# Optimization experiments

Hardware: AMD Instinct MI355X
Metric: run time of the kernel (lower is better)

## Reference

```python
import math
import jax, jax.numpy as jnp
import numpy as np

BLOCKSIZE = 1024  # Hadamard block length (power of 2, divides in_features=4096)


def fwht(x):
    """Fast Walsh-Hadamard transform over the last dim (power of 2), unnormalized.
    Iterative butterfly: H_{2h} = [[H_h, H_h], [H_h, -H_h]]."""
    n = x.shape[-1]
    steps = int(math.log2(n))
    shape = x.shape
    x = x.reshape(-1, n)
    h = 1
    for _ in range(steps):
        x = x.reshape(-1, n // (2 * h), 2, h)
        a = x[:, :, 0, :]
        b = x[:, :, 1, :]
        x = jnp.stack([a + b, a - b], axis=2).reshape(-1, n)
        h *= 2
    return x.reshape(shape)


def pad_to_block_last(x, blocksize):
    size = x.shape[-1]
    target = ((size - 1) // blocksize + 1) * blocksize
    delta = target - size
    if delta == 0:
        return x
    pad = [(0, 0)] * (x.ndim - 1) + [(0, delta)]
    return jnp.pad(x, pad)


def setup_inputs() -> dict:
    key = jax.random.key(0)
    k1, k2 = jax.random.split(key)
    x = jax.random.normal(k1, (4, 2048, 4096), dtype=jnp.float32)
    # HadLinear.__init__ divides the weight by sqrt(blocksize) when do_hadamard=True;
    # the stored parameter is the scaled weight, so we materialize it scaled.
    w = jax.random.normal(k2, (4096, 4096), dtype=jnp.float32) / math.sqrt(BLOCKSIZE)
    return {"input": x, "weight": w}


def reference(input, weight):
    bs = BLOCKSIZE
    x = pad_to_block_last(input, bs)
    lead = x.shape[:-1]
    d = x.shape[-1]
    mult = d // bs
    x = x.reshape(lead + (mult, bs))
    x = fwht(x) * (1.0 / math.sqrt(bs))  # hadamard_transform with scale=1/sqrt(bs)
    x = x.reshape(lead + (d,))
    return jnp.einsum('bsd,od->bso', x, weight)  # F.linear(x, weight)
```

## Files before the change

### kernel.cpp

```cpp
#include <hip/hip_runtime.h>
#include <hip/hip_bf16.h>
#include <cstdint>

typedef __attribute__((ext_vector_type(4))) float f32x4;
typedef __attribute__((ext_vector_type(8))) short bf16x8;
typedef unsigned short u16;

__device__ inline u16 f2b(float f) {
    union { float f; uint32_t u; } c; c.f = f;
    uint32_t r = (c.u + 0x7FFFu + ((c.u >> 16) & 1u)) >> 16;
    return (u16)r;
}

__global__ void cast_x_kernel(const float4* __restrict__ X, ushort4* __restrict__ Xb, int n4) {
    int i = blockIdx.x * blockDim.x + threadIdx.x;
    int stride = gridDim.x * blockDim.x;
    for (; i < n4; i += stride) {
        float4 v = X[i];
        ushort4 o;
        o.x = f2b(v.x); o.y = f2b(v.y); o.z = f2b(v.z); o.w = f2b(v.w);
        Xb[i] = o;
    }
}

__global__ void fwht_w_kernel(const float* __restrict__ W, u16* __restrict__ Wh) {
    __shared__ float s[1024];
    const float* src = W + (size_t)blockIdx.x * 1024;
    for (int i = threadIdx.x; i < 1024; i += 256) s[i] = src[i];
    __syncthreads();
    for (int h = 1; h < 1024; h <<= 1) {
        for (int p = threadIdx.x; p < 512; p += 256) {
            int i = ((p & ~(h - 1)) << 1) | (p & (h - 1));
            float a = s[i], b = s[i + h];
            s[i] = a + b;
            s[i + h] = a - b;
        }
        __syncthreads();
    }
    u16* dst = Wh + (size_t)blockIdx.x * 1024;
    for (int i = threadIdx.x; i < 1024; i += 256) dst[i] = f2b(s[i] * 0.03125f);
}

#define MFMA16(a, b, c) __builtin_amdgcn_mfma_f32_16x16x32_bf16(a, b, c, 0, 0, 0)

__global__ __launch_bounds__(512, 2) void gemm256_kernel(
    const u16* __restrict__ A, const u16* __restrict__ B, float* __restrict__ C,
    int M, int N, int K)
{
    __shared__ u16 lds[2][2][2][8192];

    const int tid  = threadIdx.x;
    const int wid  = tid >> 6;
    const int lane = tid & 63;
    const int wr   = wid >> 2;
    const int wc   = wid & 3;

    const int ntn = N / 256;
    const int nwg = (M / 256) * ntn;
    int bid = blockIdx.x;
    int swz = (nwg % 8 == 0) ? ((bid & 7) * (nwg >> 3) + (bid >> 3)) : bid;
    const int tm = swz / ntn, tn = swz % ntn;
    const size_t rowA0 = (size_t)tm * 256;
    const size_t rowB0 = (size_t)tn * 256;
    const int TSTEPS = K / 64;

    const int stg_row  = wid * 8 + (lane >> 3);
    const int stg_slot = (lane & 7) ^ (stg_row & 7);

    const int frow = (lane & 15) * 64;
    const int fs0  = (((lane >> 4)) ^ (lane & 7)) * 8;
    const int fs1  = ((4 + (lane >> 4)) ^ (lane & 7)) * 8;

    auto stage = [&](const u16* __restrict__ G, size_t rowbase, u16* ldsHalf, int chunk, int t) {
        int teff = t < TSTEPS ? t : TSTEPS - 1;
        const u16* g = G + (rowbase + (size_t)(chunk * 64 + stg_row)) * (size_t)K
                         + teff * 64 + stg_slot * 8;
        u16* l = ldsHalf + chunk * 4096 + wid * 512;
        __builtin_amdgcn_global_load_lds((const __attribute__((address_space(1))) void*)g,
                                         (__attribute__((address_space(3))) void*)l, 16, 0, 0);
    };

    f32x4 acc[8][4];
#pragma unroll
    for (int i = 0; i < 8; ++i)
#pragma unroll
        for (int j = 0; j < 4; ++j) acc[i][j] = (f32x4)(0.0f);

    stage(A, rowA0,       &lds[0][0][0][0], 0, 0);
    stage(A, rowA0,       &lds[0][0][0][0], 1, 0);
    stage(B, rowB0,       &lds[0][1][0][0], 0, 0);
    stage(B, rowB0,       &lds[0][1][0][0], 1, 0);
    stage(A, rowA0 + 128, &lds[0][0][1][0], 0, 0);
    stage(A, rowA0 + 128, &lds[0][0][1][0], 1, 0);
    stage(B, rowB0 + 128, &lds[0][1][1][0], 0, 0);
    stage(B, rowB0 + 128, &lds[0][1][1][0], 1, 0);
    stage(B, rowB0,       &lds[1][1][0][0], 0, 1);
    stage(B, rowB0,       &lds[1][1][0][0], 1, 1);
    stage(A, rowA0,       &lds[1][0][0][0], 0, 1);
    stage(A, rowA0,       &lds[1][0][0][0], 1, 1);
    stage(A, rowA0 + 128, &lds[1][0][1][0], 0, 1);
    stage(A, rowA0 + 128, &lds[1][0][1][0], 1, 1);
    asm volatile("s_waitcnt vmcnt(6)" ::: "memory");
    __builtin_amdgcn_s_barrier();

    for (int t = 0; t < TSTEPS; ++t) {
        const int cb = t & 1, nb = cb ^ 1;
        const u16* Ahalf = &lds[cb][0][wr][0];
        const u16* Bbase = &lds[cb][1][wc >> 1][(wc & 1) * 4096];

        bf16x8 aP[4], aQ[4], bK0[4], bK1[4];

#pragma unroll
        for (int i = 0; i < 4; ++i) aP[i]  = *(const bf16x8*)&Ahalf[i * 1024 + frow + fs0];
#pragma unroll
        for (int j = 0; j < 4; ++j) bK0[j] = *(const bf16x8*)&Bbase[j * 1024 + frow + fs0];
#pragma unroll
        for (int i = 0; i < 4; ++i) aQ[i]  = *(const bf16x8*)&Ahalf[(4 + i) * 1024 + frow + fs0];
#pragma unroll
        for (int j = 0; j < 4; ++j) bK1[j] = *(const bf16x8*)&Bbase[j * 1024 + frow + fs1];
        stage(B, rowB0 + 128, &lds[nb][1][1][0], 0, t + 1);
        stage(B, rowB0 + 128, &lds[nb][1][1][0], 1, t + 1);
        asm volatile("s_waitcnt lgkmcnt(8)" ::: "memory");
        __builtin_amdgcn_sched_barrier(0);
        __builtin_amdgcn_s_setprio(1);
#pragma unroll
        for (int i = 0; i < 4; ++i)
#pragma unroll
            for (int j = 0; j < 4; ++j)
                acc[i][j] = MFMA16(aP[i], bK0[j], acc[i][j]);
        __builtin_amdgcn_s_setprio(0);

#pragma unroll
        for (int i = 0; i < 4; ++i) aP[i] = *(const bf16x8*)&Ahalf[i * 1024 + frow + fs1];
        asm volatile("s_waitcnt lgkmcnt(4)" ::: "memory");
        __builtin_amdgcn_sched_barrier(0);
        __builtin_amdgcn_s_setprio(1);
#pragma unroll
        for (int i = 0; i < 4; ++i)
#pragma unroll
            for (int j = 0; j < 4; ++j)
                acc[4 + i][j] = MFMA16(aQ[i], bK0[j], acc[4 + i][j]);
        __builtin_amdgcn_s_setprio(0);

        __builtin_amdgcn_s_barrier();
        stage(B, rowB0, &lds[cb][1][0][0], 0, t + 2);
        stage(B, rowB0, &lds[cb][1][0][0], 1, t + 2);
#pragma unroll
        for (int i = 0; i < 4; ++i) aQ[i] = *(const bf16x8*)&Ahalf[(4 + i) * 1024 + frow + fs1];
        asm volatile("s_waitcnt lgkmcnt(4)" ::: "memory");
        __builtin_amdgcn_sched_barrier(0);
        __builtin_amdgcn_s_setprio(1);
#pragma unroll
        for (int i = 0; i < 4; ++i)
#pragma unroll
            for (int j = 0; j < 4; ++j)
                acc[i][j] = MFMA16(aP[i], bK1[j], acc[i][j]);
        __builtin_amdgcn_s_setprio(0);

        asm volatile("s_waitcnt lgkmcnt(0)" ::: "memory");
        __builtin_amdgcn_sched_barrier(0);
        __builtin_amdgcn_s_barrier();
        stage(A, rowA0,       &lds[cb][0][0][0], 0, t + 2);
        stage(A, rowA0,       &lds[cb][0][0][0], 1, t + 2);
        stage(A, rowA0 + 128, &lds[cb][0][1][0], 0, t + 2);
        stage(A, rowA0 + 128, &lds[cb][0][1][0], 1, t + 2);
        __builtin_amdgcn_s_setprio(1);
#pragma unroll
        for (int i = 0; i < 4; ++i)
#pragma unroll
            for (int j = 0; j < 4; ++j)
                acc[4 + i][j] = MFMA16(aQ[i], bK1[j], acc[4 + i][j]);
        __builtin_amdgcn_s_setprio(0);
        asm volatile("s_waitcnt vmcnt(6)" ::: "memory");
        __builtin_amdgcn_s_barrier();
    }

#pragma unroll
    for (int mf = 0; mf < 8; ++mf) {
        size_t row = rowA0 + wr * 128 + mf * 16 + (lane >> 4) * 4;
#pragma unroll
        for (int nf = 0; nf < 4; ++nf) {
            size_t col = rowB0 + wc * 64 + nf * 16 + (lane & 15);
            f32x4 v = acc[mf][nf];
#pragma unroll
            for (int j = 0; j < 4; ++j)
                C[(row + j) * (size_t)N + col] = v[j];
        }
    }
}

extern "C" void kernel_launch(void* const* d_in, const int* in_sizes, int n_in,
                              void* d_out, int out_size, void* d_ws, size_t ws_size,
                              hipStream_t stream) {
    const float* X = (const float*)d_in[0];
    const float* W = (const float*)d_in[1];
    float* Out = (float*)d_out;

    const int K = 4096;
    const int N = in_sizes[1] / K;
    const int M = in_sizes[0] / K;

    u16* Xb = (u16*)d_ws;
    u16* Wh = (u16*)d_ws + (size_t)M * K;

    cast_x_kernel<<<2048, 256, 0, stream>>>((const float4*)X, (ushort4*)Xb, (M * K) / 4);
    fwht_w_kernel<<<(size_t)N * K / 1024, 256, 0, stream>>>(W, Wh);

    dim3 grid((M / 256) * (N / 256));
    gemm256_kernel<<<grid, 512, 0, stream>>>(Xb, Wh, Out, M, N, K);
}
```

Before: 309.4 us.

## Prefetch next-tile LDS fragments across iterations and drop trailing barrier

Restructures the GEMM main loop so the first A/B fragments of the next K-step are read from LDS during the last MFMA group of the current step, which takes the initial LDS reads off the critical path at the top of each iteration. The end-of-iteration vmcnt wait plus barrier is merged into the existing mid-iteration barrier, removing one workgroup barrier per step. The prologue staging order and wait counts are also changed. This adds register pressure from the extra live fragments and makes the vmcnt bookkeeping fragile, so a miscounted wait could race on LDS.

Measured after the change: 301.1 us. 2.7% less time.

```diff
diff --git a/kernel.cpp b/kernel.cpp
--- a/kernel.cpp
+++ b/kernel.cpp
@@ -86,38 +86,46 @@
 #pragma unroll
         for (int j = 0; j < 4; ++j) acc[i][j] = (f32x4)(0.0f);
 
+    stage(B, rowB0,       &lds[0][1][0][0], 0, 0);
+    stage(B, rowB0,       &lds[0][1][0][0], 1, 0);
     stage(A, rowA0,       &lds[0][0][0][0], 0, 0);
     stage(A, rowA0,       &lds[0][0][0][0], 1, 0);
-    stage(B, rowB0,       &lds[0][1][0][0], 0, 0);
-    stage(B, rowB0,       &lds[0][1][0][0], 1, 0);
     stage(A, rowA0 + 128, &lds[0][0][1][0], 0, 0);
     stage(A, rowA0 + 128, &lds[0][0][1][0], 1, 0);
     stage(B, rowB0 + 128, &lds[0][1][1][0], 0, 0);
     stage(B, rowB0 + 128, &lds[0][1][1][0], 1, 0);
     stage(B, rowB0,       &lds[1][1][0][0], 0, 1);
     stage(B, rowB0,       &lds[1][1][0][0], 1, 1);
+    asm volatile("s_waitcnt vmcnt(2)" ::: "memory");
+    __builtin_amdgcn_s_barrier();
     stage(A, rowA0,       &lds[1][0][0][0], 0, 1);
     stage(A, rowA0,       &lds[1][0][0][0], 1, 1);
     stage(A, rowA0 + 128, &lds[1][0][1][0], 0, 1);
     stage(A, rowA0 + 128, &lds[1][0][1][0], 1, 1);
-    asm volatile("s_waitcnt vmcnt(6)" ::: "memory");
-    __builtin_amdgcn_s_barrier();
+
+    bf16x8 a0[4], b0v[4];
+    {
+        const u16* Ahalf = &lds[0][0][wr][0];
+        const u16* Bbase = &lds[0][1][wc >> 1][(wc & 1) * 4096];
+#pragma unroll
+        for (int i = 0; i < 4; ++i) a0[i]  = *(const bf16x8*)&Ahalf[i * 1024 + frow + fs0];
+#pragma unroll
+        for (int j = 0; j < 4; ++j) b0v[j] = *(const bf16x8*)&Bbase[j * 1024 + frow + fs0];
+    }
 
     for (int t = 0; t < TSTEPS; ++t) {
         const int cb = t & 1, nb = cb ^ 1;
-        const u16* Ahalf = &lds[cb][0][wr][0];
-        const u16* Bbase = &lds[cb][1][wc >> 1][(wc & 1) * 4096];
-
-        bf16x8 aP[4], aQ[4], bK0[4], bK1[4];
-
-#pragma unroll
-        for (int i = 0; i < 4; ++i) aP[i]  = *(const bf16x8*)&Ahalf[i * 1024 + frow + fs0];
-#pragma unroll
-        for (int j = 0; j < 4; ++j) bK0[j] = *(const bf16x8*)&Bbase[j * 1024 + frow + fs0];
-#pragma unroll
-        for (int i = 0; i < 4; ++i) aQ[i]  = *(const bf16x8*)&Ahalf[(4 + i) * 1024 + frow + fs0];
-#pragma unroll
-        for (int j = 0; j < 4; ++j) bK1[j] = *(const bf16x8*)&Bbase[j * 1024 + frow + fs1];
+        const u16* Ahalf  = &lds[cb][0][wr][0];
+        const u16* Bbase  = &lds[cb][1][wc >> 1][(wc & 1) * 4096];
+        const u16* AhalfN = &lds[nb][0][wr][0];
+        const u16* BbaseN = &lds[nb][1][wc >> 1][(wc & 1) * 4096];
+
+        bf16x8 a1[4], bb1[4], a2[4], a3[4];
+
+#pragma unroll
+        for (int i = 0; i < 4; ++i) a1[i]  = *(const bf16x8*)&Ahalf[(4 + i) * 1024 + frow + fs0];
+#pragma unroll
+        for (int j = 0; j < 4; ++j) bb1[j] = *(const bf16x8*)&Bbase[j * 1024 + frow + fs1];
         stage(B, rowB0 + 128, &lds[nb][1][1][0], 0, t + 1);
         stage(B, rowB0 + 128, &lds[nb][1][1][0], 1, t + 1);
         asm volatile("s_waitcnt lgkmcnt(8)" ::: "memory");
@@ -127,26 +135,26 @@
         for (int i = 0; i < 4; ++i)
 #pragma unroll
             for (int j = 0; j < 4; ++j)
-                acc[i][j] = MFMA16(aP[i], bK0[j], acc[i][j]);
-        __builtin_amdgcn_s_setprio(0);
-
-#pragma unroll
-        for (int i = 0; i < 4; ++i) aP[i] = *(const bf16x8*)&Ahalf[i * 1024 + frow + fs1];
-        asm volatile("s_waitcnt lgkmcnt(4)" ::: "memory");
-        __builtin_amdgcn_sched_barrier(0);
-        __builtin_amdgcn_s_setprio(1);
-#pragma unroll
-        for (int i = 0; i < 4; ++i)
-#pragma unroll
-            for (int j = 0; j < 4; ++j)
-                acc[4 + i][j] = MFMA16(aQ[i], bK0[j], acc[4 + i][j]);
+                acc[i][j] = MFMA16(a0[i], b0v[j], acc[i][j]);
+        __builtin_amdgcn_s_setprio(0);
+
+#pragma unroll
+        for (int i = 0; i < 4; ++i) a2[i] = *(const bf16x8*)&Ahalf[i * 1024 + frow + fs1];
+        asm volatile("s_waitcnt lgkmcnt(8)" ::: "memory");
+        __builtin_amdgcn_sched_barrier(0);
+        __builtin_amdgcn_s_setprio(1);
+#pragma unroll
+        for (int i = 0; i < 4; ++i)
+#pragma unroll
+            for (int j = 0; j < 4; ++j)
+                acc[4 + i][j] = MFMA16(a1[i], b0v[j], acc[4 + i][j]);
         __builtin_amdgcn_s_setprio(0);
 
         __builtin_amdgcn_s_barrier();
         stage(B, rowB0, &lds[cb][1][0][0], 0, t + 2);
         stage(B, rowB0, &lds[cb][1][0][0], 1, t + 2);
 #pragma unroll
-        for (int i = 0; i < 4; ++i) aQ[i] = *(const bf16x8*)&Ahalf[(4 + i) * 1024 + frow + fs1];
+        for (int i = 0; i < 4; ++i) a3[i] = *(const bf16x8*)&Ahalf[(4 + i) * 1024 + frow + fs1];
         asm volatile("s_waitcnt lgkmcnt(4)" ::: "memory");
         __builtin_amdgcn_sched_barrier(0);
         __builtin_amdgcn_s_setprio(1);
@@ -154,25 +162,28 @@
         for (int i = 0; i < 4; ++i)
 #pragma unroll
             for (int j = 0; j < 4; ++j)
-                acc[i][j] = MFMA16(aP[i], bK1[j], acc[i][j]);
+                acc[i][j] = MFMA16(a2[i], bb1[j], acc[i][j]);
         __builtin_amdgcn_s_setprio(0);
 
         asm volatile("s_waitcnt lgkmcnt(0)" ::: "memory");
+        asm volatile("s_waitcnt vmcnt(2)" ::: "memory");
         __builtin_amdgcn_sched_barrier(0);
         __builtin_amdgcn_s_barrier();
         stage(A, rowA0,       &lds[cb][0][0][0], 0, t + 2);
         stage(A, rowA0,       &lds[cb][0][0][0], 1, t + 2);
         stage(A, rowA0 + 128, &lds[cb][0][1][0], 0, t + 2);
         stage(A, rowA0 + 128, &lds[cb][0][1][0], 1, t + 2);
-        __builtin_amdgcn_s_setprio(1);
-#pragma unroll
-        for (int i = 0; i < 4; ++i)
-#pragma unroll
-            for (int j = 0; j < 4; ++j)
-                acc[4 + i][j] = MFMA16(aQ[i], bK1[j], acc[4 + i][j]);
-        __builtin_amdgcn_s_setprio(0);
-        asm volatile("s_waitcnt vmcnt(6)" ::: "memory");
-        __builtin_amdgcn_s_barrier();
+#pragma unroll
+        for (int i = 0; i < 4; ++i) a0[i]  = *(const bf16x8*)&AhalfN[i * 1024 + frow + fs0];
+#pragma unroll
+        for (int j = 0; j < 4; ++j) b0v[j] = *(const bf16x8*)&BbaseN[j * 1024 + frow + fs0];
+        __builtin_amdgcn_s_setprio(1);
+#pragma unroll
+        for (int i = 0; i < 4; ++i)
+#pragma unroll
+            for (int j = 0; j < 4; ++j)
+                acc[4 + i][j] = MFMA16(a3[i], bb1[j], acc[4 + i][j]);
+        __builtin_amdgcn_s_setprio(0);
     }
 
 #pragma unroll
```
